# Kernel optimization log

Hardware: AMD Instinct MI355X
Metric: run time of the kernel (lower is better)

Reference implementation:

```python
import jax, jax.numpy as jnp
import numpy as np

H = 1024          # en_hidden_size
NUM_LAYERS = 3
NUM_CLASS = 60
IN_SIZE = 150
EPS = 1e-5


def _gru_dir(x, w_ih, w_hh, b_ih, b_hh):
    """Single-direction GRU run forward in time. x: [N,T,in] -> [N,T,H].
    PyTorch GRU cell math."""
    gi = jnp.einsum('nti,gi->ntg', x, w_ih) + b_ih  # [N,T,3H] input projections

    def step(h, gi_t):
        gh = h @ w_hh.T + b_hh
        i_r, i_z, i_n = jnp.split(gi_t, 3, axis=-1)
        h_r, h_z, h_n = jnp.split(gh, 3, axis=-1)
        r = jax.nn.sigmoid(i_r + h_r)
        z = jax.nn.sigmoid(i_z + h_z)
        n = jnp.tanh(i_n + r * h_n)
        h_new = (1.0 - z) * n + z * h
        return h_new, h_new

    h0 = jnp.zeros((x.shape[0], H), dtype=x.dtype)
    _, ys = jax.lax.scan(step, h0, jnp.swapaxes(gi, 0, 1))  # ys: [T,N,H]
    return jnp.swapaxes(ys, 0, 1)


def _bigru_forward(x, bn_gamma, bn_beta,
                   w_ih_0, w_hh_0, b_ih_0, b_hh_0,
                   w_ih_1, w_hh_1, b_ih_1, b_hh_1,
                   w_ih_2, w_hh_2, b_ih_2, b_hh_2,
                   fc_w, fc_b):
    # BatchNorm1d (train mode): stats over (N,T) per channel, biased variance.
    mean = jnp.mean(x, axis=(0, 1), keepdims=True)
    var = jnp.mean(jnp.square(x - mean), axis=(0, 1), keepdims=True)
    h_in = (x - mean) * jax.lax.rsqrt(var + EPS) * bn_gamma + bn_beta

    # NOTE: the original advances the bidirectional GRU one timestep at a time
    # while carrying the hidden state, so BOTH directions run forward in time.
    layer_params = [(w_ih_0, w_hh_0, b_ih_0, b_hh_0),
                    (w_ih_1, w_hh_1, b_ih_1, b_hh_1),
                    (w_ih_2, w_hh_2, b_ih_2, b_hh_2)]
    for (w_ih, w_hh, b_ih, b_hh) in layer_params:
        outs = [_gru_dir(h_in, w_ih[d], w_hh[d], b_ih[d], b_hh[d]) for d in range(2)]
        h_in = jnp.concatenate(outs, axis=-1)  # [N,T,2H]

    encoder_hidden = h_in                      # [N,T,2H]
    hidden = encoder_hidden[:, -1, :]          # seq_len == T for every sample
    out = hidden @ fc_w.T + fc_b               # [N, num_class]
    return out, encoder_hidden


def setup_inputs() -> dict:
    key = jax.random.key(0)
    ks = jax.random.split(key, 32)
    N, T = 256, 64
    s = 1.0 / np.sqrt(H)
    inp = {}
    inp['x'] = jax.random.normal(ks[0], (N, T, IN_SIZE), dtype=jnp.float32)
    inp['bn_gamma'] = jnp.ones((IN_SIZE,), jnp.float32)
    inp['bn_beta'] = jnp.zeros((IN_SIZE,), jnp.float32)
    in_sizes = [IN_SIZE, 2 * H, 2 * H]
    ki = 1
    for l in range(NUM_LAYERS):
        inp[f'w_ih_{l}'] = jax.random.uniform(ks[ki], (2, 3 * H, in_sizes[l]), jnp.float32, -s, s); ki += 1
        inp[f'w_hh_{l}'] = jax.random.uniform(ks[ki], (2, 3 * H, H), jnp.float32, -s, s); ki += 1
        inp[f'b_ih_{l}'] = jax.random.uniform(ks[ki], (2, 3 * H), jnp.float32, -s, s); ki += 1
        inp[f'b_hh_{l}'] = jax.random.uniform(ks[ki], (2, 3 * H), jnp.float32, -s, s); ki += 1
    inp['fc_w'] = jax.random.uniform(ks[ki], (NUM_CLASS, 2 * H), jnp.float32, -s, s); ki += 1
    inp['fc_b'] = jax.random.uniform(ks[ki], (NUM_CLASS,), jnp.float32, -s, s)
    return inp


def reference(x, bn_gamma, bn_beta,
              w_ih_0, w_hh_0, b_ih_0, b_hh_0,
              w_ih_1, w_hh_1, b_ih_1, b_hh_1,
              w_ih_2, w_hh_2, b_ih_2, b_hh_2,
              fc_w, fc_b):
    return _bigru_forward(x, bn_gamma, bn_beta,
                          w_ih_0, w_hh_0, b_ih_0, b_hh_0,
                          w_ih_1, w_hh_1, b_ih_1, b_hh_1,
                          w_ih_2, w_hh_2, b_ih_2, b_hh_2,
                          fc_w, fc_b)
```

## Files before the change

### kernel.cpp

```cpp
#include <hip/hip_runtime.h>
#include <hip/hip_bf16.h>
#include <hip/hip_fp16.h>
#include <math.h>

#define HH    1024
#define TT    64
#define NBAT  256
#define G3    3072
#define IN0   150
#define IN0P  160
#define NCLS  60
#define ENC_W 2048

typedef float  f32x4 __attribute__((ext_vector_type(4)));
typedef short  s16x8 __attribute__((ext_vector_type(8)));

#define GLOAD16(gsrc, ldst) \
  __builtin_amdgcn_global_load_lds((const __attribute__((address_space(1))) unsigned int*)(gsrc), \
                                   (__attribute__((address_space(3))) unsigned int*)(ldst), 16, 0, 0)

static __device__ inline short f2bf(float f) {
    __hip_bfloat16 h = __float2bfloat16(f);
    return *(short*)&h;
}

__global__ void bigru_bn_stats(const float* __restrict__ x,
                               float* __restrict__ mean, float* __restrict__ istd) {
    int f = blockIdx.x;
    int tid = threadIdx.x;
    double s = 0.0, s2 = 0.0;
    for (int i = tid; i < NBAT * TT; i += blockDim.x) {
        float v = x[(size_t)i * IN0 + f];
        s += v; s2 += (double)v * v;
    }
    __shared__ double sh[256], sh2[256];
    sh[tid] = s; sh2[tid] = s2;
    __syncthreads();
    for (int off = 128; off > 0; off >>= 1) {
        if (tid < off) { sh[tid] += sh[tid + off]; sh2[tid] += sh2[tid + off]; }
        __syncthreads();
    }
    if (tid == 0) {
        double m = sh[0] / (NBAT * TT);
        double var = sh2[0] / (NBAT * TT) - m * m;
        mean[f] = (float)m;
        istd[f] = (float)(1.0 / sqrt(var + 1e-5));
    }
}

__global__ void bigru_bn_apply_bf16(const float* __restrict__ x,
                                    const float* __restrict__ mean, const float* __restrict__ istd,
                                    const float* __restrict__ gamma, const float* __restrict__ beta,
                                    short* __restrict__ xn) {
    int idx = blockIdx.x * blockDim.x + threadIdx.x;
    if (idx >= NBAT * TT * IN0P) return;
    int f = idx % IN0P;
    int r = idx / IN0P;
    float v = 0.f;
    if (f < IN0) v = (x[(size_t)r * IN0 + f] - mean[f]) * istd[f] * gamma[f] + beta[f];
    xn[idx] = f2bf(v);
}

__global__ void bigru_cvt_wih0(const float* __restrict__ src, short* __restrict__ dst) {
    int idx = blockIdx.x * blockDim.x + threadIdx.x;
    if (idx >= 2 * G3 * IN0P) return;
    int f = idx % IN0P;
    int r = idx / IN0P;
    float v = (f < IN0) ? src[(size_t)r * IN0 + f] : 0.f;
    dst[idx] = f2bf(v);
}

__global__ void bigru_cvt4(const float* __restrict__ src, short* __restrict__ dst, int n4) {
    int i = blockIdx.x * blockDim.x + threadIdx.x;
    if (i >= n4) return;
    float4 v = ((const float4*)src)[i];
    short4 o;
    o.x = f2bf(v.x); o.y = f2bf(v.y); o.z = f2bf(v.z); o.w = f2bf(v.w);
    ((short4*)dst)[i] = o;
}

__global__ __launch_bounds__(256)
void bigru_gi_gemm(const short* __restrict__ Abase, int ldA, int K,
                   const short* __restrict__ W,
                   const float* __restrict__ b_ih,
                   __half* __restrict__ gi,
                   int t0, int Mchunk) {
    int d    = blockIdx.z;
    int col0 = blockIdx.x * 128;
    int row0 = blockIdx.y * 128;

    __shared__ short As[128][32];
    __shared__ short Bs[128][32];

    int tid  = threadIdx.x;
    int lane = tid & 63;
    int w    = tid >> 6;
    int wm   = w & 1, wn = w >> 1;

    f32x4 acc[4][4];
    #pragma unroll
    for (int i = 0; i < 4; ++i)
        #pragma unroll
        for (int j = 0; j < 4; ++j)
            acc[i][j] = (f32x4){0.f, 0.f, 0.f, 0.f};

    const short* Wd = W + (size_t)d * G3 * K;
    int sr = lane >> 2;
    int sc = (lane & 3) * 8;

    for (int k0 = 0; k0 < K; k0 += 32) {
        #pragma unroll
        for (int q = 0; q < 2; ++q) {
            int r  = w * 32 + q * 16 + sr;
            int gr = row0 + r;
            int tt = gr >> 8, n = gr & 255;
            const short* ga = Abase + (size_t)(n * TT + t0 + tt) * ldA + k0 + sc;
            GLOAD16(ga, &As[w * 32 + q * 16][0]);
            const short* gb = Wd + (size_t)(col0 + r) * K + k0 + sc;
            GLOAD16(gb, &Bs[w * 32 + q * 16][0]);
        }
        __syncthreads();

        int fr = lane & 15, fq = (lane >> 4) * 8;
        s16x8 a[4], b[4];
        #pragma unroll
        for (int i = 0; i < 4; ++i) a[i] = *(const s16x8*)&As[wm * 64 + i * 16 + fr][fq];
        #pragma unroll
        for (int j = 0; j < 4; ++j) b[j] = *(const s16x8*)&Bs[wn * 64 + j * 16 + fr][fq];
        #pragma unroll
        for (int i = 0; i < 4; ++i)
            #pragma unroll
            for (int j = 0; j < 4; ++j)
                acc[i][j] = __builtin_amdgcn_mfma_f32_16x16x32_bf16(a[i], b[j], acc[i][j], 0, 0, 0);
        __syncthreads();
    }

    int fr = lane & 15, quad = lane >> 4;
    #pragma unroll
    for (int j = 0; j < 4; ++j) {
        int c = col0 + wn * 64 + j * 16 + fr;
        float bias = b_ih[d * G3 + c];
        #pragma unroll
        for (int i = 0; i < 4; ++i) {
            #pragma unroll
            for (int reg = 0; reg < 4; ++reg) {
                int r = row0 + wm * 64 + i * 16 + quad * 4 + reg;
                gi[((size_t)d * Mchunk + r) * G3 + c] = __float2half(acc[i][j][reg] + bias);
            }
        }
    }
}

__global__ __launch_bounds__(256, 1)
void bigru_step(const short* __restrict__ w_hh,
                const float* __restrict__ b_hh,
                const __half* __restrict__ gi,
                float* __restrict__ h,
                const short* __restrict__ hbf_in,
                short* __restrict__ hbf_out,
                float* __restrict__ enc,
                short* __restrict__ enc_bf,
                int t, int ttl, int Mchunk) {
    __shared__ short Ws[48 * 1024];
    __shared__ short As[4][4][1024];

    int b   = blockIdx.x;
    int d   = b & 1;
    int mt  = (b >> 1) & 1;
    int ct  = b >> 2;

    int tid  = threadIdx.x;
    int lane = tid & 63;
    int w    = tid >> 6;
    int fr   = lane & 15;
    int quad = lane >> 4;
    int sw   = fr & 7;

    int j0 = ct * 16;
    int row_base = mt * 128 + w * 32;
    int jcol = j0 + fr;

    const short* Wd = w_hh + (size_t)d * G3 * HH;

    #pragma unroll
    for (int q = 0; q < 24; ++q) {
        int c  = w * 24 + q;
        int rr = c >> 1, kh = c & 1;
        int g  = rr >> 4, jc = rr & 15;
        const short* src = Wd + (size_t)(g * HH + j0 + jc) * HH
                         + (size_t)(kh * 64 + (lane ^ (rr & 7))) * 8;
        GLOAD16(src, &Ws[rr * 1024 + kh * 512]);
    }

    int l0 = lane & 1, l1 = (lane >> 1) & 1, l2 = (lane >> 2) & 1;
    int l3 = (lane >> 3) & 1, l4 = (lane >> 4) & 1, l5 = (lane >> 5) & 1;
    int arow = (l2 ^ l4) | (l3 << 1) | (l4 << 2) | (l5 << 3);
    int akb  = (l0 ^ l2 ^ l4) | ((l1 ^ l3) << 1);
    const short* hb = hbf_in + (size_t)d * NBAT * HH;
    const short* asrc0 = hb + (size_t)(row_base + arow) * HH + (size_t)akb * 8;
    const short* asrc1 = hb + (size_t)(row_base + 16 + arow) * HH + (size_t)akb * 8;

    float gir[2][4], giz[2][4], gin[2][4], hreg[2][4];
    {
        size_t gb = ((size_t)d * Mchunk + (size_t)ttl * NBAT) * G3 + jcol;
        #pragma unroll
        for (int hh = 0; hh < 2; ++hh)
            #pragma unroll
            for (int r = 0; r < 4; ++r) {
                int n = row_base + hh * 16 + quad * 4 + r;
                size_t gg = gb + (size_t)n * G3;
                gir[hh][r] = __half2float(gi[gg]);
                giz[hh][r] = __half2float(gi[gg + HH]);
                gin[hh][r] = __half2float(gi[gg + 2 * HH]);
                hreg[hh][r] = h[((size_t)d * NBAT + n) * HH + jcol];
            }
    }
    float bhr = b_hh[d * G3 + jcol];
    float bhz = b_hh[d * G3 + HH + jcol];
    float bhn = b_hh[d * G3 + 2 * HH + jcol];

    __syncthreads();

    f32x4 acc[2][3];
    #pragma unroll
    for (int hh = 0; hh < 2; ++hh)
        #pragma unroll
        for (int g = 0; g < 3; ++g)
            acc[hh][g] = (f32x4){0.f, 0.f, 0.f, 0.f};

    #pragma unroll
    for (int c = 0; c < 3; ++c) {
        GLOAD16(asrc0 + c * 32, &As[w][c][0]);
        GLOAD16(asrc1 + c * 32, &As[w][c][512]);
    }

    int rd_off = (fr * 64 + quad * 16) ^ ((fr & 7) << 4);

    #pragma unroll
    for (int c = 0; c < 32; ++c) {
        if (c < 30)       asm volatile("s_waitcnt vmcnt(4)");
        else if (c == 30) asm volatile("s_waitcnt vmcnt(2)");
        else              asm volatile("s_waitcnt vmcnt(0)");
        __builtin_amdgcn_sched_barrier(0);
        const char* slot = (const char*)&As[w][c & 3][0];
        s16x8 a0 = *(const s16x8*)(slot + rd_off);
        s16x8 a1 = *(const s16x8*)(slot + 1024 + rd_off);
        int ks = c * 4 + quad;
        #pragma unroll
        for (int g = 0; g < 3; ++g) {
            s16x8 bg = *(const s16x8*)&Ws[(g * 16 + fr) * 1024 + ((ks ^ sw) << 3)];
            acc[0][g] = __builtin_amdgcn_mfma_f32_16x16x32_bf16(a0, bg, acc[0][g], 0, 0, 0);
            acc[1][g] = __builtin_amdgcn_mfma_f32_16x16x32_bf16(a1, bg, acc[1][g], 0, 0, 0);
        }
        __builtin_amdgcn_sched_barrier(0);
        if (c + 3 < 32) {
            GLOAD16(asrc0 + (c + 3) * 32, &As[w][(c + 3) & 3][0]);
            GLOAD16(asrc1 + (c + 3) * 32, &As[w][(c + 3) & 3][512]);
        }
    }

    short* ho = hbf_out + (size_t)d * NBAT * HH;
    #pragma unroll
    for (int hh = 0; hh < 2; ++hh) {
        #pragma unroll
        for (int r = 0; r < 4; ++r) {
            int n = row_base + hh * 16 + quad * 4 + r;
            float hrv = acc[hh][0][r] + bhr;
            float hzv = acc[hh][1][r] + bhz;
            float hnv = acc[hh][2][r] + bhn;
            float rg = 1.f / (1.f + __expf(-(gir[hh][r] + hrv)));
            float zg = 1.f / (1.f + __expf(-(giz[hh][r] + hzv)));
            float ng = tanhf(gin[hh][r] + rg * hnv);
            float hnew = (1.f - zg) * ng + zg * hreg[hh][r];
            h[((size_t)d * NBAT + n) * HH + jcol] = hnew;
            ho[(size_t)n * HH + jcol] = f2bf(hnew);
            size_t eidx = ((size_t)n * TT + t) * ENC_W + (size_t)d * HH + jcol;
            if (enc_bf) enc_bf[eidx] = f2bf(hnew);
            if (enc)    enc[eidx]    = hnew;
        }
    }
}

__global__ void bigru_fc(const float* __restrict__ enc, const float* __restrict__ fc_w,
                         const float* __restrict__ fc_b, float* __restrict__ out) {
    int n = blockIdx.x;
    int tid = threadIdx.x;
    __shared__ float hbuf[ENC_W];
    for (int k = tid; k < ENC_W; k += blockDim.x)
        hbuf[k] = enc[(size_t)n * TT * ENC_W + (size_t)(TT - 1) * ENC_W + k];
    __syncthreads();
    if (tid < NCLS) {
        float acc = fc_b[tid];
        for (int k = 0; k < ENC_W; ++k)
            acc += hbuf[k] * fc_w[(size_t)tid * ENC_W + k];
        out[(size_t)n * NCLS + tid] = acc;
    }
}

extern "C" void kernel_launch(void* const* d_in, const int* in_sizes, int n_in,
                              void* d_out, int out_size, void* d_ws, size_t ws_size,
                              hipStream_t stream) {
    const float* x        = (const float*)d_in[0];
    const float* bn_gamma = (const float*)d_in[1];
    const float* bn_beta  = (const float*)d_in[2];
    const float* w_ih[3]  = {(const float*)d_in[3], (const float*)d_in[7],  (const float*)d_in[11]};
    const float* w_hh[3]  = {(const float*)d_in[4], (const float*)d_in[8],  (const float*)d_in[12]};
    const float* b_ih[3]  = {(const float*)d_in[5], (const float*)d_in[9],  (const float*)d_in[13]};
    const float* b_hh[3]  = {(const float*)d_in[6], (const float*)d_in[10], (const float*)d_in[14]};
    const float* fc_w     = (const float*)d_in[15];
    const float* fc_b     = (const float*)d_in[16];

    float* out = (float*)d_out;
    float* enc = out + NBAT * NCLS;

    char* base = (char*)d_ws;
    size_t off = 0;
    auto alloc = [&](size_t bytes) {
        void* p = base + off;
        off += (bytes + 255) & ~(size_t)255;
        return p;
    };
    float* mean      = (float*)alloc(IN0 * 4);
    float* istd      = (float*)alloc(IN0 * 4);
    short* xn_bf     = (short*)alloc((size_t)NBAT * TT * IN0P * 2);
    short* wih0_bf   = (short*)alloc((size_t)2 * G3 * IN0P * 2);
    short* wih_bf    = (short*)alloc((size_t)2 * G3 * ENC_W * 2);
    short* whh_bf    = (short*)alloc((size_t)2 * G3 * HH * 2);
    float* h         = (float*)alloc((size_t)2 * NBAT * HH * 4);
    short* hbf       = (short*)alloc((size_t)2 * 2 * NBAT * HH * 2);
    short* enc_bf    = (short*)alloc((size_t)NBAT * TT * ENC_W * 2);
    size_t fixed = off;

    int Tc = 1;
    for (int cand : {16, 8, 4, 2, 1}) {
        size_t gi_bytes = (size_t)2 * NBAT * cand * G3 * 2;
        if (fixed + gi_bytes + 1024 <= ws_size) { Tc = cand; break; }
    }
    __half* gi = (__half*)alloc((size_t)2 * NBAT * Tc * G3 * 2);
    int Mchunk = NBAT * Tc;

    bigru_bn_stats<<<IN0, 256, 0, stream>>>(x, mean, istd);
    bigru_bn_apply_bf16<<<(NBAT * TT * IN0P + 255) / 256, 256, 0, stream>>>(
        x, mean, istd, bn_gamma, bn_beta, xn_bf);

    bigru_cvt_wih0<<<(2 * G3 * IN0P + 255) / 256, 256, 0, stream>>>(w_ih[0], wih0_bf);

    for (int l = 0; l < 3; ++l) {
        if (l > 0) {
            int n4 = (2 * G3 * ENC_W) / 4;
            bigru_cvt4<<<(n4 + 255) / 256, 256, 0, stream>>>(w_ih[l], wih_bf, n4);
        }
        {
            int n4 = (2 * G3 * HH) / 4;
            bigru_cvt4<<<(n4 + 255) / 256, 256, 0, stream>>>(w_hh[l], whh_bf, n4);
        }
        hipMemsetAsync(h, 0, (size_t)2 * NBAT * HH * 4, stream);
        hipMemsetAsync(hbf, 0, (size_t)2 * 2 * NBAT * HH * 2, stream);

        const short* Abase = (l == 0) ? xn_bf : enc_bf;
        int ldA = (l == 0) ? IN0P : ENC_W;
        int K   = (l == 0) ? IN0P : ENC_W;
        const short* W = (l == 0) ? wih0_bf : wih_bf;
        float* enc_out   = (l == 2) ? enc : nullptr;
        short* encbf_out = (l == 2) ? nullptr : enc_bf;

        for (int t0 = 0; t0 < TT; t0 += Tc) {
            bigru_gi_gemm<<<dim3(G3 / 128, Mchunk / 128, 2), 256, 0, stream>>>(
                Abase, ldA, K, W, b_ih[l], gi, t0, Mchunk);

            for (int tt = 0; tt < Tc; ++tt) {
                int t = t0 + tt;
                const short* hin = hbf + (size_t)(t & 1) * 2 * NBAT * HH;
                short*       hout = hbf + (size_t)((t + 1) & 1) * 2 * NBAT * HH;
                bigru_step<<<dim3(256), 256, 0, stream>>>(
                    whh_bf, b_hh[l], gi, h, hin, hout,
                    enc_out, encbf_out, t, tt, Mchunk);
            }
        }
    }

    bigru_fc<<<NBAT, 256, 0, stream>>>(enc, fc_w, fc_b, out);
}
```

Measured before the change: 4.301 ms.

## Restructure GRU step: 512-thread blocks, register-resident h tile, two column passes

The recurrent step kernel now uses 128 blocks of 512 threads. Each wave holds its 16-row slice of the hidden state in registers (32 bf16x8 fragments) instead of streaming it through an LDS ring buffer with manual vmcnt waits. Each block covers 32 hidden columns in two sequential passes, reloading the W_hh slice into LDS between them. This gives each W_hh load more reuse, halves the grid and removes the LDS staging for h. The cost is high register pressure (128 VGPRs for areg, under a 512,2 launch bound), a serialized second weight load with extra syncthreads, and fewer blocks than CUs.

```diff
diff --git a/kernel.cpp b/kernel.cpp
--- a/kernel.cpp
+++ b/kernel.cpp
@@ -151,7 +151,7 @@
     }
 }
 
-__global__ __launch_bounds__(256, 1)
+__global__ __launch_bounds__(512, 2)
 void bigru_step(const short* __restrict__ w_hh,
                 const float* __restrict__ b_hh,
                 const __half* __restrict__ gi,
@@ -162,12 +162,11 @@
                 short* __restrict__ enc_bf,
                 int t, int ttl, int Mchunk) {
     __shared__ short Ws[48 * 1024];
-    __shared__ short As[4][4][1024];
 
     int b   = blockIdx.x;
     int d   = b & 1;
     int mt  = (b >> 1) & 1;
-    int ct  = b >> 2;
+    int cg  = b >> 2;
 
     int tid  = threadIdx.x;
     int lane = tid & 63;
@@ -176,15 +175,15 @@
     int quad = lane >> 4;
     int sw   = fr & 7;
 
-    int j0 = ct * 16;
-    int row_base = mt * 128 + w * 32;
-    int jcol = j0 + fr;
+    int j0 = cg * 32;
+    int row_base = mt * 128 + w * 16;
 
     const short* Wd = w_hh + (size_t)d * G3 * HH;
-
-    #pragma unroll
-    for (int q = 0; q < 24; ++q) {
-        int c  = w * 24 + q;
+    const short* hb = hbf_in + (size_t)d * NBAT * HH;
+
+    #pragma unroll
+    for (int q = 0; q < 12; ++q) {
+        int c  = w * 12 + q;
         int rr = c >> 1, kh = c & 1;
         int g  = rr >> 4, jc = rr & 15;
         const short* src = Wd + (size_t)(g * HH + j0 + jc) * HH
@@ -192,86 +191,89 @@
         GLOAD16(src, &Ws[rr * 1024 + kh * 512]);
     }
 
-    int l0 = lane & 1, l1 = (lane >> 1) & 1, l2 = (lane >> 2) & 1;
-    int l3 = (lane >> 3) & 1, l4 = (lane >> 4) & 1, l5 = (lane >> 5) & 1;
-    int arow = (l2 ^ l4) | (l3 << 1) | (l4 << 2) | (l5 << 3);
-    int akb  = (l0 ^ l2 ^ l4) | ((l1 ^ l3) << 1);
-    const short* hb = hbf_in + (size_t)d * NBAT * HH;
-    const short* asrc0 = hb + (size_t)(row_base + arow) * HH + (size_t)akb * 8;
-    const short* asrc1 = hb + (size_t)(row_base + 16 + arow) * HH + (size_t)akb * 8;
+    const short* asrc = hb + (size_t)(row_base + fr) * HH + quad * 8;
+    s16x8 areg[32];
+    #pragma unroll
+    for (int c = 0; c < 32; ++c)
+        areg[c] = *(const s16x8*)(asrc + c * 32);
 
     float gir[2][4], giz[2][4], gin[2][4], hreg[2][4];
-    {
+    float bhr[2], bhz[2], bhn[2];
+    #pragma unroll
+    for (int p = 0; p < 2; ++p) {
+        int jcol = j0 + p * 16 + fr;
+        bhr[p] = b_hh[d * G3 + jcol];
+        bhz[p] = b_hh[d * G3 + HH + jcol];
+        bhn[p] = b_hh[d * G3 + 2 * HH + jcol];
         size_t gb = ((size_t)d * Mchunk + (size_t)ttl * NBAT) * G3 + jcol;
         #pragma unroll
-        for (int hh = 0; hh < 2; ++hh)
-            #pragma unroll
-            for (int r = 0; r < 4; ++r) {
-                int n = row_base + hh * 16 + quad * 4 + r;
-                size_t gg = gb + (size_t)n * G3;
-                gir[hh][r] = __half2float(gi[gg]);
-                giz[hh][r] = __half2float(gi[gg + HH]);
-                gin[hh][r] = __half2float(gi[gg + 2 * HH]);
-                hreg[hh][r] = h[((size_t)d * NBAT + n) * HH + jcol];
-            }
-    }
-    float bhr = b_hh[d * G3 + jcol];
-    float bhz = b_hh[d * G3 + HH + jcol];
-    float bhn = b_hh[d * G3 + 2 * HH + jcol];
-
-    __syncthreads();
+        for (int r = 0; r < 4; ++r) {
+            int n = row_base + quad * 4 + r;
+            size_t gg = gb + (size_t)n * G3;
+            gir[p][r] = __half2float(gi[gg]);
+            giz[p][r] = __half2float(gi[gg + HH]);
+            gin[p][r] = __half2float(gi[gg + 2 * HH]);
+            hreg[p][r] = h[((size_t)d * NBAT + n) * HH + jcol];
+        }
+    }
 
     f32x4 acc[2][3];
     #pragma unroll
-    for (int hh = 0; hh < 2; ++hh)
+    for (int p = 0; p < 2; ++p)
         #pragma unroll
         for (int g = 0; g < 3; ++g)
-            acc[hh][g] = (f32x4){0.f, 0.f, 0.f, 0.f};
-
-    #pragma unroll
-    for (int c = 0; c < 3; ++c) {
-        GLOAD16(asrc0 + c * 32, &As[w][c][0]);
-        GLOAD16(asrc1 + c * 32, &As[w][c][512]);
-    }
-
-    int rd_off = (fr * 64 + quad * 16) ^ ((fr & 7) << 4);
+            acc[p][g] = (f32x4){0.f, 0.f, 0.f, 0.f};
+
+    __syncthreads();
 
     #pragma unroll
     for (int c = 0; c < 32; ++c) {
-        if (c < 30)       asm volatile("s_waitcnt vmcnt(4)");
-        else if (c == 30) asm volatile("s_waitcnt vmcnt(2)");
-        else              asm volatile("s_waitcnt vmcnt(0)");
-        __builtin_amdgcn_sched_barrier(0);
-        const char* slot = (const char*)&As[w][c & 3][0];
-        s16x8 a0 = *(const s16x8*)(slot + rd_off);
-        s16x8 a1 = *(const s16x8*)(slot + 1024 + rd_off);
         int ks = c * 4 + quad;
         #pragma unroll
         for (int g = 0; g < 3; ++g) {
             s16x8 bg = *(const s16x8*)&Ws[(g * 16 + fr) * 1024 + ((ks ^ sw) << 3)];
-            acc[0][g] = __builtin_amdgcn_mfma_f32_16x16x32_bf16(a0, bg, acc[0][g], 0, 0, 0);
-            acc[1][g] = __builtin_amdgcn_mfma_f32_16x16x32_bf16(a1, bg, acc[1][g], 0, 0, 0);
-        }
-        __builtin_amdgcn_sched_barrier(0);
-        if (c + 3 < 32) {
-            GLOAD16(asrc0 + (c + 3) * 32, &As[w][(c + 3) & 3][0]);
-            GLOAD16(asrc1 + (c + 3) * 32, &As[w][(c + 3) & 3][512]);
+            acc[0][g] = __builtin_amdgcn_mfma_f32_16x16x32_bf16(areg[c], bg, acc[0][g], 0, 0, 0);
+        }
+    }
+
+    __syncthreads();
+
+    #pragma unroll
+    for (int q = 0; q < 12; ++q) {
+        int c  = w * 12 + q;
+        int rr = c >> 1, kh = c & 1;
+        int g  = rr >> 4, jc = rr & 15;
+        const short* src = Wd + (size_t)(g * HH + j0 + 16 + jc) * HH
+                         + (size_t)(kh * 64 + (lane ^ (rr & 7))) * 8;
+        GLOAD16(src, &Ws[rr * 1024 + kh * 512]);
+    }
+
+    __syncthreads();
+
+    #pragma unroll
+    for (int c = 0; c < 32; ++c) {
+        int ks = c * 4 + quad;
+        #pragma unroll
+        for (int g = 0; g < 3; ++g) {
+            s16x8 bg = *(const s16x8*)&Ws[(g * 16 + fr) * 1024 + ((ks ^ sw) << 3)];
+            acc[1][g] = __builtin_amdgcn_mfma_f32_16x16x32_bf16(areg[c], bg, acc[1][g], 0, 0, 0);
         }
     }
 
     short* ho = hbf_out + (size_t)d * NBAT * HH;
     #pragma unroll
-    for (int hh = 0; hh < 2; ++hh) {
+    for (int p = 0; p < 2; ++p) {
+        int jcol = j0 + p * 16 + fr;
         #pragma unroll
         for (int r = 0; r < 4; ++r) {
-            int n = row_base + hh * 16 + quad * 4 + r;
-            float hrv = acc[hh][0][r] + bhr;
-            float hzv = acc[hh][1][r] + bhz;
-            float hnv = acc[hh][2][r] + bhn;
-            float rg = 1.f / (1.f + __expf(-(gir[hh][r] + hrv)));
-            float zg = 1.f / (1.f + __expf(-(giz[hh][r] + hzv)));
-            float ng = tanhf(gin[hh][r] + rg * hnv);
-            float hnew = (1.f - zg) * ng + zg * hreg[hh][r];
+            int n = row_base + quad * 4 + r;
+            float hrv = acc[p][0][r] + bhr[p];
+            float hzv = acc[p][1][r] + bhz[p];
+            float hnv = acc[p][2][r] + bhn[p];
+            float rg = 1.f / (1.f + __expf(-(gir[p][r] + hrv)));
+            float zg = 1.f / (1.f + __expf(-(giz[p][r] + hzv)));
+            float ng = tanhf(gin[p][r] + rg * hnv);
+            float hnew = (1.f - zg) * ng + zg * hreg[p][r];
             h[((size_t)d * NBAT + n) * HH + jcol] = hnew;
             ho[(size_t)n * HH + jcol] = f2bf(hnew);
             size_t eidx = ((size_t)n * TT + t) * ENC_W + (size_t)d * HH + jcol;
@@ -372,7 +374,7 @@
                 int t = t0 + tt;
                 const short* hin = hbf + (size_t)(t & 1) * 2 * NBAT * HH;
                 short*       hout = hbf + (size_t)((t + 1) & 1) * 2 * NBAT * HH;
-                bigru_step<<<dim3(256), 256, 0, stream>>>(
+                bigru_step<<<dim3(128), 512, 0, stream>>>(
                     whh_bf, b_hh[l], gi, h, hin, hout,
                     enc_out, encbf_out, t, tt, Mchunk);
             }
```

New measurement: 8.767 ms. 104% more time.
